# Kernel optimization log

Hardware: AMD Instinct MI355X
Metric: run time of the kernel (lower is better)

## Reference

```python
import jax, jax.numpy as jnp
import numpy as np
from jax import lax

EPS = 1e-5

def _conv(x, w, pad):
    # x: NCHW, w: OIHW, stride 1
    return lax.conv_general_dilated(x, w, (1, 1), [(pad, pad), (pad, pad)],
                                    dimension_numbers=('NCHW', 'OIHW', 'NCHW'))

def _binconv(x, w):
    # IR-Net/ReActNet HardBinaryConv: sign-binarized weights scaled by per-filter
    # mean |w| (alpha), sign-binarized activations; clip-based STE for backward.
    alpha = jnp.mean(jnp.abs(w), axis=(1, 2, 3), keepdims=True)  # [O,1,1,1]
    wc = jnp.clip(w, -1.0, 1.0)
    bw = lax.stop_gradient(alpha * jnp.sign(w) - wc) + wc
    xc = jnp.clip(x, -1.0, 1.0)
    ba = lax.stop_gradient(jnp.sign(x) - xc) + xc
    return _conv(ba, bw, 1)

def _bn(x, g, b, m, v):
    # inference-mode BatchNorm2d with running stats
    inv = g / jnp.sqrt(v + EPS)
    return x * inv[None, :, None, None] + (b - m * inv)[None, :, None, None]

def _pool(x):
    return lax.reduce_window(x, -jnp.inf, lax.max, (1, 1, 2, 2), (1, 1, 2, 2), 'VALID')

def _htanh(x):
    return jnp.clip(x, -1.0, 1.0)

def setup_inputs() -> dict:
    key = jax.random.key(0)
    ks = jax.random.split(key, 40)
    B = 256
    d = {'x': jax.random.normal(ks[0], (B, 3, 32, 32), jnp.float32)}
    shapes = [(128, 3, 3, 3), (128, 128, 3, 3), (256, 128, 3, 3),
              (256, 256, 3, 3), (512, 256, 3, 3), (512, 512, 3, 3)]
    chans = [128, 128, 256, 256, 512, 512]
    ki = 1
    for i, (ws, c) in enumerate(zip(shapes, chans)):
        fan_in = ws[1] * 9
        d[f'w{i}'] = jax.random.normal(ks[ki], ws, jnp.float32) / np.sqrt(fan_in); ki += 1
        d[f'g{i}'] = jnp.ones((c,), jnp.float32)
        d[f'b{i}'] = jnp.zeros((c,), jnp.float32)
        d[f'm{i}'] = jax.random.normal(ks[ki], (c,), jnp.float32) * 0.1; ki += 1
        d[f'v{i}'] = jax.random.uniform(ks[ki], (c,), jnp.float32, 0.5, 1.5); ki += 1
    d['fcw'] = jax.random.normal(ks[ki], (10, 512 * 4 * 4), jnp.float32) * 0.01
    d['fcb'] = jnp.zeros((10,), jnp.float32)
    return d

def reference(x, w0, g0, b0, m0, v0, w1, g1, b1, m1, v1, w2, g2, b2, m2, v2,
              w3, g3, b3, m3, v3, w4, g4, b4, m4, v4, w5, g5, b5, m5, v5,
              fcw, fcb):
    h = _bn(_conv(x, w0, 1), g0, b0, m0, v0)            # [B,128,32,32]
    h = _htanh(_bn(_pool(_binconv(h, w1)), g1, b1, m1, v1))   # [B,128,16,16]
    h = _htanh(_bn(_binconv(h, w2), g2, b2, m2, v2))          # [B,256,16,16]
    h = _htanh(_bn(_pool(_binconv(h, w3)), g3, b3, m3, v3))   # [B,256,8,8]
    h = _htanh(_bn(_binconv(h, w4), g4, b4, m4, v4))          # [B,512,8,8]
    h = _htanh(_bn(_pool(_binconv(h, w5)), g5, b5, m5, v5))   # [B,512,4,4]
    h = h.reshape(h.shape[0], -1)                             # [B,8192]
    return h @ fcw.T + fcb                                    # [B,10]
```

## Files before the change

### kernel.cpp

```cpp
#include <hip/hip_runtime.h>
#include <cstdint>

#define EPS 1e-5
typedef unsigned long long u64;
typedef unsigned int u32;

struct BnArgs { const float *g[6], *b[6], *m[6], *v[6]; };
struct PackArgs { const float* w[5]; u64* wb[5]; };

__global__ void bn_prep_all(BnArgs p, double* __restrict__ scale_all,
                            double* __restrict__ shift_all) {
    int i = blockIdx.x * 256 + threadIdx.x;
    if (i >= 1792) return;
    int l, base;
    if (i < 128)       { l = 0; base = 0; }
    else if (i < 256)  { l = 1; base = 128; }
    else if (i < 512)  { l = 2; base = 256; }
    else if (i < 768)  { l = 3; base = 512; }
    else if (i < 1280) { l = 4; base = 768; }
    else               { l = 5; base = 1280; }
    const int c = i - base;
    double inv = (double)p.g[l][c] / sqrt((double)p.v[l][c] + EPS);
    scale_all[i] = inv;
    shift_all[i] = (double)p.b[l][c] - (double)p.m[l][c] * inv;
}

__global__ void zero_out(float* __restrict__ out, int n) {
    int i = blockIdx.x * blockDim.x + threadIdx.x;
    if (i < n) out[i] = 0.f;
}

__global__ void pack_all(PackArgs pk, const double* __restrict__ scale_all,
                         double* __restrict__ A_all) {
    const int ob = blockIdx.x;
    const int t = threadIdx.x;
    int l, base, Cin, bnoff;
    if (ob < 128)       { l = 0; base = 0;    Cin = 128; bnoff = 128; }
    else if (ob < 384)  { l = 1; base = 128;  Cin = 128; bnoff = 256; }
    else if (ob < 640)  { l = 2; base = 384;  Cin = 256; bnoff = 512; }
    else if (ob < 1152) { l = 3; base = 640;  Cin = 256; bnoff = 768; }
    else                { l = 4; base = 1152; Cin = 512; bnoff = 1280; }
    const int o = ob - base;
    const float* wo = pk.w[l] + (size_t)o * Cin * 9;

    double s = 0.0;
    for (int k = t; k < Cin * 9; k += 256) s += fabs((double)wo[k]);
    __shared__ double red[256];
    red[t] = s;
    __syncthreads();
    for (int r = 128; r > 0; r >>= 1) {
        if (t < r) red[t] += red[t + r];
        __syncthreads();
    }
    if (t == 0) {
        double alpha = red[0] / (double)(Cin * 9);
        A_all[ob] = alpha * scale_all[bnoff + o];
    }

    const int W64 = Cin / 64;
    u64* wb = pk.wb[l];
    for (int e = t; e < 9 * W64; e += 256) {
        int tap = e / W64, word = e % W64;
        u64 bits = 0;
        for (int j = 0; j < 64; ++j) {
            int c = word * 64 + j;
            if (wo[c * 9 + tap] < 0.f) bits |= (1ull << j);
        }
        wb[((size_t)o * 9 + tap) * W64 + word] = bits;
    }
}

__global__ __launch_bounds__(256) void conv0_pack(
        const float* __restrict__ x, const float* __restrict__ w0,
        const double* __restrict__ scale, const double* __restrict__ shift,
        u64* __restrict__ bits0) {
    __shared__ double wlds[128 * 27];
    __shared__ double sc[128], sh[128];
    const int tid = threadIdx.x;
    for (int e = tid; e < 128 * 27; e += 256) wlds[e] = (double)w0[e];
    for (int e = tid; e < 128; e += 256) { sc[e] = scale[e]; sh[e] = shift[e]; }
    __syncthreads();

    const int n = blockIdx.y;
    const int p = blockIdx.x * 256 + tid;
    const int y = p >> 5, xx = p & 31;
    const float* xn = x + (size_t)n * 3 * 32 * 32;

    double win[27];
#pragma unroll
    for (int c = 0; c < 3; ++c)
#pragma unroll
        for (int dy = 0; dy < 3; ++dy)
#pragma unroll
            for (int dx = 0; dx < 3; ++dx) {
                const int yy = y + dy - 1, xs = xx + dx - 1;
                const bool ok = (yy >= 0 && yy < 32 && xs >= 0 && xs < 32);
                win[(c * 3 + dy) * 3 + dx] = ok ? (double)xn[(c * 32 + yy) * 32 + xs] : 0.0;
            }

    u64* op = bits0 + ((size_t)n * 1024 + p) * 2;
#pragma unroll
    for (int og = 0; og < 2; ++og) {
        u64 word = 0;
#pragma unroll 2
        for (int j = 0; j < 64; ++j) {
            const int o = og * 64 + j;
            const double* wo = &wlds[o * 27];
            double acc = 0.0;
#pragma unroll
            for (int k = 0; k < 27; ++k) acc = fma(wo[k], win[k], acc);
            const double val = acc * sc[o] + sh[o];
            word |= (u64)(val < 0.0) << j;
        }
        op[og] = word;
    }
}

template<int H, int W, int W64, int OTOT, int OPW>
__global__ __launch_bounds__(256) void bconv_np(
        const u64* __restrict__ in_bits, const u64* __restrict__ wb,
        const double* __restrict__ A, const double* __restrict__ B,
        u32* __restrict__ out_bits) {
    const int tid = threadIdx.x;
    const int wave = tid >> 6, lane = tid & 63;
    constexpr int WPI = (H * W) / 64;
    constexpr int IPB = 4 / WPI;
    const int img = blockIdx.y * IPB + (IPB == 1 ? 0 : wave);
    const int pw  = (IPB == 1 ? wave : 0);
    const int p = pw * 64 + lane;
    const int y = p / W, x = p % W;
    const int obase = blockIdx.x * OPW;

    __shared__ u64 wlds[OPW * 9 * W64];
    __shared__ double Alds[OPW], Blds[OPW];
    {
        const u64* wg = wb + (size_t)obase * 9 * W64;
        for (int e = tid; e < OPW * 9 * W64; e += 256) wlds[e] = wg[e];
        for (int e = tid; e < OPW; e += 256) { Alds[e] = A[obase + e]; Blds[e] = B[obase + e]; }
    }
    __syncthreads();

    const u64* ib = in_bits + (size_t)img * H * W * W64;
    u64 win[3][3][W64];
    bool tv[3][3];
    int nvalid = 0;
#pragma unroll
    for (int dy = 0; dy < 3; ++dy)
#pragma unroll
        for (int dx = 0; dx < 3; ++dx) {
            const int yy = y + dy - 1, xs = x + dx - 1;
            const bool ok = (yy >= 0 && yy < H && xs >= 0 && xs < W);
            tv[dy][dx] = ok;
            nvalid += ok ? 1 : 0;
            const u64* q = ib + ((size_t)yy * W + xs) * W64;
#pragma unroll
            for (int k = 0; k < W64; ++k) win[dy][dx][k] = ok ? q[k] : 0ull;
        }
    const int basev = nvalid * 64 * W64;

    u32 obuf[OPW / 32];
    u32 cur = 0;
    for (int oc = 0; oc < OPW; ++oc) {
        const u64* wo = &wlds[oc * 9 * W64];
        int pop = 0;
#pragma unroll
        for (int dy = 0; dy < 3; ++dy)
#pragma unroll
            for (int dx = 0; dx < 3; ++dx) {
                int tp = 0;
#pragma unroll
                for (int k = 0; k < W64; ++k)
                    tp += (int)__popcll(win[dy][dx][k] ^ wo[(dy * 3 + dx) * W64 + k]);
                pop += tv[dy][dx] ? tp : 0;
            }
        const int v = basev - 2 * pop;
        const double t = fma(Alds[oc], (double)v, Blds[oc]);
        cur |= (u32)(t < 0.0) << (oc & 31);
        if ((oc & 31) == 31) { obuf[oc >> 5] = cur; cur = 0; }
    }
    u32* op = out_bits + ((size_t)img * H * W + (size_t)y * W + x) * (OTOT / 32) + (obase >> 5);
#pragma unroll
    for (int j = 0; j < OPW / 32; ++j) op[j] = obuf[j];
}

template<int H, int W, int W64, int OTOT, int OPW>
__global__ __launch_bounds__(256) void bconv_pl(
        const u64* __restrict__ in_bits, const u64* __restrict__ wb,
        const double* __restrict__ A, const double* __restrict__ B,
        u32* __restrict__ out_bits) {
    const int tid = threadIdx.x;
    const int wave = tid >> 6, lane = tid & 63;
    constexpr int Hp = H / 2, Wp = W / 2;
    constexpr int WPI = (Hp * Wp) / 64;
    constexpr int IPB = 4 / WPI;
    const int img = blockIdx.y * IPB + (IPB == 1 ? 0 : wave);
    const int pw  = (IPB == 1 ? wave : 0);
    const int p = pw * 64 + lane;
    const int py = p / Wp, px = p % Wp;
    const int obase = blockIdx.x * OPW;

    __shared__ u64 wlds[OPW * 9 * W64];
    __shared__ double Alds[OPW], Blds[OPW];
    {
        const u64* wg = wb + (size_t)obase * 9 * W64;
        for (int e = tid; e < OPW * 9 * W64; e += 256) wlds[e] = wg[e];
        for (int e = tid; e < OPW; e += 256) { Alds[e] = A[obase + e]; Blds[e] = B[obase + e]; }
    }
    __syncthreads();

    const u64* ib = in_bits + (size_t)img * H * W * W64;
    u64 win[4][4][W64];
    bool wv[4][4];
#pragma unroll
    for (int wy = 0; wy < 4; ++wy)
#pragma unroll
        for (int wx = 0; wx < 4; ++wx) {
            const int yy = 2 * py - 1 + wy, xs = 2 * px - 1 + wx;
            const bool ok = (yy >= 0 && yy < H && xs >= 0 && xs < W);
            wv[wy][wx] = ok;
            const u64* q = ib + ((size_t)yy * W + xs) * W64;
#pragma unroll
            for (int k = 0; k < W64; ++k) win[wy][wx][k] = ok ? q[k] : 0ull;
        }
    int nv[2][2];
#pragma unroll
    for (int pp = 0; pp < 2; ++pp)
#pragma unroll
        for (int qq = 0; qq < 2; ++qq) {
            int c = 0;
#pragma unroll
            for (int dy = 0; dy < 3; ++dy)
#pragma unroll
                for (int dx = 0; dx < 3; ++dx) c += wv[pp + dy][qq + dx] ? 1 : 0;
            nv[pp][qq] = c * 64 * W64;
        }

    u32 obuf[OPW / 32];
    u32 cur = 0;
    for (int oc = 0; oc < OPW; ++oc) {
        const u64* wo = &wlds[oc * 9 * W64];
        int pop[2][2] = {{0, 0}, {0, 0}};
#pragma unroll
        for (int dy = 0; dy < 3; ++dy)
#pragma unroll
            for (int dx = 0; dx < 3; ++dx) {
                u64 wk[W64];
#pragma unroll
                for (int k = 0; k < W64; ++k) wk[k] = wo[(dy * 3 + dx) * W64 + k];
#pragma unroll
                for (int pp = 0; pp < 2; ++pp)
#pragma unroll
                    for (int qq = 0; qq < 2; ++qq) {
                        int tp = 0;
#pragma unroll
                        for (int k = 0; k < W64; ++k)
                            tp += (int)__popcll(win[pp + dy][qq + dx][k] ^ wk[k]);
                        pop[pp][qq] += wv[pp + dy][qq + dx] ? tp : 0;
                    }
            }
        int v = nv[0][0] - 2 * pop[0][0];
        v = max(v, nv[0][1] - 2 * pop[0][1]);
        v = max(v, nv[1][0] - 2 * pop[1][0]);
        v = max(v, nv[1][1] - 2 * pop[1][1]);
        const double t = fma(Alds[oc], (double)v, Blds[oc]);
        cur |= (u32)(t < 0.0) << (oc & 31);
        if ((oc & 31) == 31) { obuf[oc >> 5] = cur; cur = 0; }
    }
    u32* op = out_bits + ((size_t)img * Hp * Wp + (size_t)py * Wp + px) * (OTOT / 32) + (obase >> 5);
#pragma unroll
    for (int j = 0; j < OPW / 32; ++j) op[j] = obuf[j];
}

template<int OPW>
__global__ __launch_bounds__(256) void bconv_last(
        const u64* __restrict__ in_bits, const u64* __restrict__ wb,
        const double* __restrict__ A, const double* __restrict__ B,
        float* __restrict__ h5) {
    constexpr int H = 8, W = 8, W64 = 8, OTOT = 512;
    const int tid = threadIdx.x;
    const int wave = tid >> 6, lane = tid & 63;
    const int img = blockIdx.y * 4 + wave;
    const int y = lane >> 3, x = lane & 7;
    const int obase = blockIdx.x * OPW;

    __shared__ u64 wlds[OPW * 9 * W64];
    __shared__ double Alds[OPW], Blds[OPW];
    {
        const u64* wg = wb + (size_t)obase * 9 * W64;
        for (int e = tid; e < OPW * 9 * W64; e += 256) wlds[e] = wg[e];
        for (int e = tid; e < OPW; e += 256) { Alds[e] = A[obase + e]; Blds[e] = B[obase + e]; }
    }
    __syncthreads();

    const u64* ib = in_bits + (size_t)img * H * W * W64;
    u64 win[3][3][W64];
    bool tv[3][3];
    int nvalid = 0;
#pragma unroll
    for (int dy = 0; dy < 3; ++dy)
#pragma unroll
        for (int dx = 0; dx < 3; ++dx) {
            const int yy = y + dy - 1, xs = x + dx - 1;
            const bool ok = (yy >= 0 && yy < H && xs >= 0 && xs < W);
            tv[dy][dx] = ok;
            nvalid += ok ? 1 : 0;
            const u64* q = ib + ((size_t)yy * W + xs) * W64;
#pragma unroll
            for (int k = 0; k < W64; ++k) win[dy][dx][k] = ok ? q[k] : 0ull;
        }
    const int basev = nvalid * 64 * W64;
    const bool writer = ((lane & 1) == 0) && ((lane & 8) == 0);
    const int py = lane >> 4, px = (lane & 7) >> 1;

    for (int oc = 0; oc < OPW; ++oc) {
        const u64* wo = &wlds[oc * 9 * W64];
        int pop = 0;
#pragma unroll
        for (int dy = 0; dy < 3; ++dy)
#pragma unroll
            for (int dx = 0; dx < 3; ++dx) {
                int tp = 0;
#pragma unroll
                for (int k = 0; k < W64; ++k)
                    tp += (int)__popcll(win[dy][dx][k] ^ wo[(dy * 3 + dx) * W64 + k]);
                pop += tv[dy][dx] ? tp : 0;
            }
        const int v = basev - 2 * pop;
        int v2 = max(v, __shfl_xor(v, 1, 64));
        int v4 = max(v2, __shfl_xor(v2, 8, 64));
        const double t = fma(Alds[oc], (double)v4, Blds[oc]);
        const double hcl = fmin(1.0, fmax(-1.0, t));
        if (writer)
            h5[(((size_t)img * OTOT + obase + oc) * 4 + py) * 4 + px] = (float)hcl;
    }
}

__global__ void fc_kernel(const float* __restrict__ h, const float* __restrict__ fcw,
                          const float* __restrict__ fcb, float* __restrict__ out) {
    const int n = blockIdx.x, t = threadIdx.x;
    double acc[10];
#pragma unroll
    for (int j = 0; j < 10; ++j) acc[j] = 0.0;
    const float* hn = h + (size_t)n * 8192;
    for (int k = t; k < 8192; k += 256) {
        double xv = (double)hn[k];
#pragma unroll
        for (int j = 0; j < 10; ++j) acc[j] += xv * (double)fcw[j * 8192 + k];
    }
    __shared__ double red[10][256];
#pragma unroll
    for (int j = 0; j < 10; ++j) red[j][t] = acc[j];
    __syncthreads();
    for (int r = 128; r > 0; r >>= 1) {
        if (t < r) {
#pragma unroll
            for (int j = 0; j < 10; ++j) red[j][t] += red[j][t + r];
        }
        __syncthreads();
    }
    if (t < 10) out[n * 10 + t] = (float)(red[t][0] + (double)fcb[t]);
}

extern "C" void kernel_launch(void* const* d_in, const int* in_sizes, int n_in,
                              void* d_out, int out_size, void* d_ws, size_t ws_size,
                              hipStream_t stream) {
    const float* X = (const float*)d_in[0];
    BnArgs bn;
    PackArgs pk;
    const float* Wt0 = (const float*)d_in[1];
    for (int i = 0; i < 6; ++i) {
        bn.g[i] = (const float*)d_in[2 + 5 * i];
        bn.b[i] = (const float*)d_in[3 + 5 * i];
        bn.m[i] = (const float*)d_in[4 + 5 * i];
        bn.v[i] = (const float*)d_in[5 + 5 * i];
    }
    for (int i = 0; i < 5; ++i) pk.w[i] = (const float*)d_in[1 + 5 * (i + 1)];
    const float* fcw = (const float*)d_in[31];
    const float* fcb = (const float*)d_in[32];
    float* out = (float*)d_out;

    char* ws = (char*)d_ws;
    size_t off = 0;
    auto alloc = [&](size_t bytes) -> void* {
        void* p = ws + off;
        off = (off + bytes + 255) & ~(size_t)255;
        return p;
    };

    double* scale_all = (double*)alloc(1792 * sizeof(double));
    double* shift_all = (double*)alloc(1792 * sizeof(double));
    double* A_all     = (double*)alloc(1664 * sizeof(double));
    const size_t WBN[5] = {128ull * 9 * 2, 256ull * 9 * 2, 256ull * 9 * 4,
                           512ull * 9 * 4, 512ull * 9 * 8};
    for (int i = 0; i < 5; ++i) pk.wb[i] = (u64*)alloc(WBN[i] * sizeof(u64));
    u64* bits0 = (u64*)alloc(256ull * 32 * 32 * 2 * sizeof(u64));
    u64* bits1 = (u64*)alloc(256ull * 16 * 16 * 2 * sizeof(u64));
    u64* bits2 = (u64*)alloc(256ull * 16 * 16 * 4 * sizeof(u64));
    u64* bits3 = (u64*)alloc(256ull * 8 * 8 * 4 * sizeof(u64));
    u64* bits4 = (u64*)alloc(256ull * 8 * 8 * 8 * sizeof(u64));
    float* h5  = (float*)alloc(256ull * 8192 * sizeof(float));

    if (off > ws_size) {
        zero_out<<<dim3((out_size + 255) / 256), dim3(256), 0, stream>>>(out, out_size);
        return;
    }

    const int BOF[6] = {0, 128, 256, 512, 768, 1280};
    const int AOF[5] = {0, 128, 384, 640, 1152};

    bn_prep_all<<<dim3(7), dim3(256), 0, stream>>>(bn, scale_all, shift_all);
    pack_all<<<dim3(1664), dim3(256), 0, stream>>>(pk, scale_all, A_all);

    conv0_pack<<<dim3(4, 256), dim3(256), 0, stream>>>(
        X, Wt0, scale_all + BOF[0], shift_all + BOF[0], bits0);

    bconv_pl<32, 32, 2, 128, 64><<<dim3(2, 256), dim3(256), 0, stream>>>(
        bits0, pk.wb[0], A_all + AOF[0], shift_all + BOF[1], (u32*)bits1);
    bconv_np<16, 16, 2, 256, 128><<<dim3(2, 256), dim3(256), 0, stream>>>(
        bits1, pk.wb[1], A_all + AOF[1], shift_all + BOF[2], (u32*)bits2);
    bconv_pl<16, 16, 4, 256, 32><<<dim3(8, 64), dim3(256), 0, stream>>>(
        bits2, pk.wb[2], A_all + AOF[2], shift_all + BOF[3], (u32*)bits3);
    bconv_np<8, 8, 4, 512, 64><<<dim3(8, 64), dim3(256), 0, stream>>>(
        bits3, pk.wb[3], A_all + AOF[3], shift_all + BOF[4], (u32*)bits4);
    bconv_last<64><<<dim3(8, 64), dim3(256), 0, stream>>>(
        bits4, pk.wb[4], A_all + AOF[4], shift_all + BOF[5], h5);

    fc_kernel<<<dim3(256), dim3(256), 0, stream>>>(h5, fcw, fcb, out);
}
```

Before: 650.8 us.

## Map pooled binary convs to one lane per pre-pool pixel with shuffle max-pool

Replaces the 4x4-window pooled binary conv kernel, where each thread computed four conv outputs, with a generalized version of the last-layer kernel. Now one lane computes one pre-pool pixel and the 2x2 max is formed through lane shuffles. The same kernel handles both the packed-bit output and the final float output. This gives four times more threads per layer and lighter register windows, in exchange for redundant popcount work per pooled output and idle non-writer lanes during stores. It also adds min-waves launch bounds and halves the output-channels-per-block in several layers to raise occupancy and grid size.

```diff
diff --git a/kernel.cpp b/kernel.cpp
--- a/kernel.cpp
+++ b/kernel.cpp
@@ -116,17 +116,17 @@
     }
 }
 
-template<int H, int W, int W64, int OTOT, int OPW>
-__global__ __launch_bounds__(256) void bconv_np(
+template<int H, int W, int W64, int OTOT, int OPW, int MINW>
+__global__ __launch_bounds__(256, MINW) void bconv_np(
         const u64* __restrict__ in_bits, const u64* __restrict__ wb,
         const double* __restrict__ A, const double* __restrict__ B,
         u32* __restrict__ out_bits) {
     const int tid = threadIdx.x;
     const int wave = tid >> 6, lane = tid & 63;
     constexpr int WPI = (H * W) / 64;
-    constexpr int IPB = 4 / WPI;
-    const int img = blockIdx.y * IPB + (IPB == 1 ? 0 : wave);
-    const int pw  = (IPB == 1 ? wave : 0);
+    constexpr int IPB = (WPI >= 4) ? 1 : 4 / WPI;
+    const int img = (IPB == 1) ? blockIdx.y : blockIdx.y * IPB + wave;
+    const int pw  = (IPB == 1) ? wave : 0;
     const int p = pw * 64 + lane;
     const int y = p / W, x = p % W;
     const int obase = blockIdx.x * OPW;
@@ -183,21 +183,22 @@
     for (int j = 0; j < OPW / 32; ++j) op[j] = obuf[j];
 }
 
-template<int H, int W, int W64, int OTOT, int OPW>
-__global__ __launch_bounds__(256) void bconv_pl(
+template<int H, int W, int W64, int OTOT, int OPW, int MINW, bool LAST>
+__global__ __launch_bounds__(256, MINW) void bconv_ps(
         const u64* __restrict__ in_bits, const u64* __restrict__ wb,
         const double* __restrict__ A, const double* __restrict__ B,
-        u32* __restrict__ out_bits) {
+        u32* __restrict__ out_bits, float* __restrict__ h5) {
     const int tid = threadIdx.x;
     const int wave = tid >> 6, lane = tid & 63;
+    constexpr int RPW = 64 / W;
+    constexpr int WPI = (H * W) / 64;
+    constexpr int IPB = (WPI >= 4) ? 1 : 4 / WPI;
+    const int img = (IPB == 1) ? blockIdx.z : blockIdx.z * IPB + wave;
+    const int wii = (IPB == 1) ? blockIdx.y * 4 + wave : 0;
+    const int y = wii * RPW + lane / W;
+    const int x = lane % W;
+    const int obase = blockIdx.x * OPW;
     constexpr int Hp = H / 2, Wp = W / 2;
-    constexpr int WPI = (Hp * Wp) / 64;
-    constexpr int IPB = 4 / WPI;
-    const int img = blockIdx.y * IPB + (IPB == 1 ? 0 : wave);
-    const int pw  = (IPB == 1 ? wave : 0);
-    const int p = pw * 64 + lane;
-    const int py = p / Wp, px = p % Wp;
-    const int obase = blockIdx.x * OPW;
 
     __shared__ u64 wlds[OPW * 9 * W64];
     __shared__ double Alds[OPW], Blds[OPW];
@@ -209,90 +210,6 @@
     __syncthreads();
 
     const u64* ib = in_bits + (size_t)img * H * W * W64;
-    u64 win[4][4][W64];
-    bool wv[4][4];
-#pragma unroll
-    for (int wy = 0; wy < 4; ++wy)
-#pragma unroll
-        for (int wx = 0; wx < 4; ++wx) {
-            const int yy = 2 * py - 1 + wy, xs = 2 * px - 1 + wx;
-            const bool ok = (yy >= 0 && yy < H && xs >= 0 && xs < W);
-            wv[wy][wx] = ok;
-            const u64* q = ib + ((size_t)yy * W + xs) * W64;
-#pragma unroll
-            for (int k = 0; k < W64; ++k) win[wy][wx][k] = ok ? q[k] : 0ull;
-        }
-    int nv[2][2];
-#pragma unroll
-    for (int pp = 0; pp < 2; ++pp)
-#pragma unroll
-        for (int qq = 0; qq < 2; ++qq) {
-            int c = 0;
-#pragma unroll
-            for (int dy = 0; dy < 3; ++dy)
-#pragma unroll
-                for (int dx = 0; dx < 3; ++dx) c += wv[pp + dy][qq + dx] ? 1 : 0;
-            nv[pp][qq] = c * 64 * W64;
-        }
-
-    u32 obuf[OPW / 32];
-    u32 cur = 0;
-    for (int oc = 0; oc < OPW; ++oc) {
-        const u64* wo = &wlds[oc * 9 * W64];
-        int pop[2][2] = {{0, 0}, {0, 0}};
-#pragma unroll
-        for (int dy = 0; dy < 3; ++dy)
-#pragma unroll
-            for (int dx = 0; dx < 3; ++dx) {
-                u64 wk[W64];
-#pragma unroll
-                for (int k = 0; k < W64; ++k) wk[k] = wo[(dy * 3 + dx) * W64 + k];
-#pragma unroll
-                for (int pp = 0; pp < 2; ++pp)
-#pragma unroll
-                    for (int qq = 0; qq < 2; ++qq) {
-                        int tp = 0;
-#pragma unroll
-                        for (int k = 0; k < W64; ++k)
-                            tp += (int)__popcll(win[pp + dy][qq + dx][k] ^ wk[k]);
-                        pop[pp][qq] += wv[pp + dy][qq + dx] ? tp : 0;
-                    }
-            }
-        int v = nv[0][0] - 2 * pop[0][0];
-        v = max(v, nv[0][1] - 2 * pop[0][1]);
-        v = max(v, nv[1][0] - 2 * pop[1][0]);
-        v = max(v, nv[1][1] - 2 * pop[1][1]);
-        const double t = fma(Alds[oc], (double)v, Blds[oc]);
-        cur |= (u32)(t < 0.0) << (oc & 31);
-        if ((oc & 31) == 31) { obuf[oc >> 5] = cur; cur = 0; }
-    }
-    u32* op = out_bits + ((size_t)img * Hp * Wp + (size_t)py * Wp + px) * (OTOT / 32) + (obase >> 5);
-#pragma unroll
-    for (int j = 0; j < OPW / 32; ++j) op[j] = obuf[j];
-}
-
-template<int OPW>
-__global__ __launch_bounds__(256) void bconv_last(
-        const u64* __restrict__ in_bits, const u64* __restrict__ wb,
-        const double* __restrict__ A, const double* __restrict__ B,
-        float* __restrict__ h5) {
-    constexpr int H = 8, W = 8, W64 = 8, OTOT = 512;
-    const int tid = threadIdx.x;
-    const int wave = tid >> 6, lane = tid & 63;
-    const int img = blockIdx.y * 4 + wave;
-    const int y = lane >> 3, x = lane & 7;
-    const int obase = blockIdx.x * OPW;
-
-    __shared__ u64 wlds[OPW * 9 * W64];
-    __shared__ double Alds[OPW], Blds[OPW];
-    {
-        const u64* wg = wb + (size_t)obase * 9 * W64;
-        for (int e = tid; e < OPW * 9 * W64; e += 256) wlds[e] = wg[e];
-        for (int e = tid; e < OPW; e += 256) { Alds[e] = A[obase + e]; Blds[e] = B[obase + e]; }
-    }
-    __syncthreads();
-
-    const u64* ib = in_bits + (size_t)img * H * W * W64;
     u64 win[3][3][W64];
     bool tv[3][3];
     int nvalid = 0;
@@ -309,9 +226,11 @@
             for (int k = 0; k < W64; ++k) win[dy][dx][k] = ok ? q[k] : 0ull;
         }
     const int basev = nvalid * 64 * W64;
-    const bool writer = ((lane & 1) == 0) && ((lane & 8) == 0);
-    const int py = lane >> 4, px = (lane & 7) >> 1;
-
+    const bool writer = ((lane & 1) == 0) && ((lane & W) == 0);
+    const int py = y >> 1, px = x >> 1;
+
+    u32 obuf[OPW / 32];
+    u32 cur = 0;
     for (int oc = 0; oc < OPW; ++oc) {
         const u64* wo = &wlds[oc * 9 * W64];
         int pop = 0;
@@ -327,11 +246,22 @@
             }
         const int v = basev - 2 * pop;
         int v2 = max(v, __shfl_xor(v, 1, 64));
-        int v4 = max(v2, __shfl_xor(v2, 8, 64));
-        const double t = fma(Alds[oc], (double)v4, Blds[oc]);
-        const double hcl = fmin(1.0, fmax(-1.0, t));
-        if (writer)
-            h5[(((size_t)img * OTOT + obase + oc) * 4 + py) * 4 + px] = (float)hcl;
+        int v4 = max(v2, __shfl_xor(v2, W, 64));
+        if (LAST) {
+            const double t = fma(Alds[oc], (double)v4, Blds[oc]);
+            const double hcl = fmin(1.0, fmax(-1.0, t));
+            if (writer)
+                h5[(((size_t)img * OTOT + obase + oc) * Hp + py) * Wp + px] = (float)hcl;
+        } else {
+            const double t = fma(Alds[oc], (double)v4, Blds[oc]);
+            cur |= (u32)(t < 0.0) << (oc & 31);
+            if ((oc & 31) == 31) { obuf[oc >> 5] = cur; cur = 0; }
+        }
+    }
+    if (!LAST && writer) {
+        u32* op = out_bits + ((size_t)img * Hp * Wp + (size_t)py * Wp + px) * (OTOT / 32) + (obase >> 5);
+#pragma unroll
+        for (int j = 0; j < OPW / 32; ++j) op[j] = obuf[j];
     }
 }
 
@@ -414,16 +344,16 @@
     conv0_pack<<<dim3(4, 256), dim3(256), 0, stream>>>(
         X, Wt0, scale_all + BOF[0], shift_all + BOF[0], bits0);
 
-    bconv_pl<32, 32, 2, 128, 64><<<dim3(2, 256), dim3(256), 0, stream>>>(
-        bits0, pk.wb[0], A_all + AOF[0], shift_all + BOF[1], (u32*)bits1);
-    bconv_np<16, 16, 2, 256, 128><<<dim3(2, 256), dim3(256), 0, stream>>>(
+    bconv_ps<32, 32, 2, 128, 64, 4, false><<<dim3(2, 4, 256), dim3(256), 0, stream>>>(
+        bits0, pk.wb[0], A_all + AOF[0], shift_all + BOF[1], (u32*)bits1, nullptr);
+    bconv_np<16, 16, 2, 256, 64, 4><<<dim3(4, 256), dim3(256), 0, stream>>>(
         bits1, pk.wb[1], A_all + AOF[1], shift_all + BOF[2], (u32*)bits2);
-    bconv_pl<16, 16, 4, 256, 32><<<dim3(8, 64), dim3(256), 0, stream>>>(
-        bits2, pk.wb[2], A_all + AOF[2], shift_all + BOF[3], (u32*)bits3);
-    bconv_np<8, 8, 4, 512, 64><<<dim3(8, 64), dim3(256), 0, stream>>>(
+    bconv_ps<16, 16, 4, 256, 32, 3, false><<<dim3(8, 1, 256), dim3(256), 0, stream>>>(
+        bits2, pk.wb[2], A_all + AOF[2], shift_all + BOF[3], (u32*)bits3, nullptr);
+    bconv_np<8, 8, 4, 512, 32, 3><<<dim3(16, 64), dim3(256), 0, stream>>>(
         bits3, pk.wb[3], A_all + AOF[3], shift_all + BOF[4], (u32*)bits4);
-    bconv_last<64><<<dim3(8, 64), dim3(256), 0, stream>>>(
-        bits4, pk.wb[4], A_all + AOF[4], shift_all + BOF[5], h5);
+    bconv_ps<8, 8, 8, 512, 32, 2, true><<<dim3(16, 1, 64), dim3(256), 0, stream>>>(
+        bits4, pk.wb[4], A_all + AOF[4], shift_all + BOF[5], nullptr, h5);
 
     fc_kernel<<<dim3(256), dim3(256), 0, stream>>>(h5, fcw, fcb, out);
 }
```

Result: faster. 608.6 us (-6.5%).
